# Kernel optimization log

Hardware: AMD Instinct MI355X
Metric: run time of the kernel (lower is better)

The kernel has to match this reference:

```python
import jax, jax.numpy as jnp
import numpy as np

N = 648      # code length (input_size = output_size)
DV = 3       # variable degree
DC = 6       # check degree
M_PER = N // DC            # checks per layer = 108
E = N * DV                 # edges = hidden_size = 1944
BATCH = 2048
CLAMP = 0.999999


def _build_graph():
    rng = np.random.default_rng(0)
    # regular (3,6) Tanner graph via 3 permutation layers
    var_of = np.concatenate([rng.permutation(N) for _ in range(DV)])          # [E]
    chk_of = np.repeat(np.arange(DV * M_PER), DC)                              # [E]
    eye = np.eye(E, dtype=bool)
    same_chk = (chk_of[:, None] == chk_of[None, :]) & ~eye                     # extrinsic same-check
    same_var = (var_of[:, None] == var_of[None, :]) & ~eye                     # extrinsic same-var
    M_ev = np.zeros((E, N), dtype=np.float32)
    M_ev[np.arange(E), var_of] = 1.0                                           # edge -> its variable
    M_first = (same_chk.astype(np.float32) @ M_ev)                             # [E,N] CN extrinsic over vars
    M_cn = same_chk.astype(np.float32)                                         # [E,E] VN2CN_mask_CNUpdate
    M_vn = same_var.astype(np.float32)                                         # [E,E] CN2VN_mask_VNUpdate
    M_out = M_ev.T.copy()                                                      # [N,E] CN2VN_mask_output
    bias_matrix = M_ev.T.copy()                                                # [N,E] dot_bias_matrix
    return M_first, M_cn, M_vn, M_out, bias_matrix


def _xavier(key, out_f, in_f, mask):
    bound = np.sqrt(6.0 / (in_f + out_f)).astype(np.float32)
    w = jax.random.uniform(key, (out_f, in_f), jnp.float32, -bound, bound)
    return w * mask


def setup_inputs() -> dict:
    key = jax.random.key(0)
    M_first, M_cn, M_vn, M_out, bias_matrix = _build_graph()
    M_first = jnp.asarray(M_first); M_cn = jnp.asarray(M_cn)
    M_vn = jnp.asarray(M_vn); M_out = jnp.asarray(M_out)
    bias_matrix = jnp.asarray(bias_matrix)
    ks = jax.random.split(key, 6)
    x = jax.random.normal(ks[0], (BATCH, N), jnp.float32) * 2.0  # channel LLRs
    W1 = _xavier(ks[1], E, E, M_vn)
    W3 = _xavier(ks[2], E, E, M_vn)
    W5 = _xavier(ks[3], E, E, M_vn)
    W7 = _xavier(ks[4], E, E, M_vn)
    W9 = _xavier(ks[5], N, E, M_out)
    B0 = jnp.eye(N, dtype=jnp.float32); B1 = jnp.eye(N, dtype=jnp.float32)
    B2 = jnp.eye(N, dtype=jnp.float32); B3 = jnp.eye(N, dtype=jnp.float32)
    B4 = jnp.eye(N, dtype=jnp.float32)
    return {"x": x, "M_first": M_first, "M_cn": M_cn, "M_out": M_out,
            "bias_matrix": bias_matrix, "W1": W1, "W3": W3, "W5": W5,
            "W7": W7, "W9": W9, "B0": B0, "B1": B1, "B2": B2, "B3": B3, "B4": B4}


def cn_update(x, mask):
    """out[b,i] = prod over j with mask[i,j]!=0 and x[b,j]!=0 of x[b,j]; 0 if none.
    Computed in sign/log domain so it is three dense [B,in]@[in,out] matmuls
    instead of a Python loop over rows."""
    nz = x != 0.0
    logmag = jnp.log(jnp.where(nz, jnp.abs(x), 1.0))          # 0 contribution where x==0
    neg = (x < 0.0).astype(x.dtype)
    log_prod = logmag @ mask.T                                 # [B,out]
    neg_cnt = neg @ mask.T
    sign = 1.0 - 2.0 * jnp.mod(neg_cnt, 2.0)
    any_nz = (nz.astype(x.dtype) @ mask.T) > 0.0
    return jnp.where(any_nz, sign * jnp.exp(log_prod), 0.0)


def reference(x, M_first, M_cn, M_out, bias_matrix, W1, W3, W5, W7, W9,
              B0, B1, B2, B3, B4):
    llr = x                                                    # Channel_LLR [B,N]
    t = jnp.tanh(0.5 * x)
    t = jnp.clip(cn_update(t, M_first), -CLAMP, CLAMP)
    t = 2.0 * jnp.arctanh(t)
    out1 = jax.nn.sigmoid(t @ M_out.T + llr)                   # count_loss_fc: ones*mask weight, zero bias

    t = jnp.tanh(0.5 * (t @ W1.T + (llr @ B0) @ bias_matrix))
    t = jnp.clip(cn_update(t, M_cn), -CLAMP, CLAMP)
    t = 2.0 * jnp.arctanh(t)
    out2 = jax.nn.sigmoid(t @ M_out.T + llr)

    t = jnp.tanh(0.5 * (t @ W3.T + (llr @ B1) @ bias_matrix))
    t = jnp.clip(cn_update(t, M_cn), -CLAMP, CLAMP)
    t = 2.0 * jnp.arctanh(t)
    out3 = jax.nn.sigmoid(t @ M_out.T + llr)

    t = jnp.tanh(0.5 * (t @ W5.T + (llr @ B2) @ bias_matrix))
    t = jnp.clip(cn_update(t, M_cn), -CLAMP, CLAMP)
    t = 2.0 * jnp.arctanh(t)
    out4 = jax.nn.sigmoid(t @ M_out.T + llr)

    t = jnp.tanh(0.5 * (t @ W7.T + (llr @ B3) @ bias_matrix))
    t = jnp.clip(cn_update(t, M_cn), -CLAMP, CLAMP)
    t = 2.0 * jnp.arctanh(t)
    t = t @ W9.T + llr @ B4
    out5 = jax.nn.sigmoid(t)
    return (out5, out4, out3, out2, out1)
```

## Files before the change

kernel.cpp:

```cpp
#include <hip/hip_runtime.h>
#include <math.h>

#define NN 648
#define EE 1944
#define NCHK 324
#define BATCH 2048
#define BS 256
#define BSM 384
#define ROWS 2
#define TL_CLAMP 14.508648f

__device__ __forceinline__ float rcp_fast(float x) { return __builtin_amdgcn_rcpf(x); }

__device__ __forceinline__ float tanh_half(float x) {
    float E = __expf(x);
    float big = 1.0f - 2.0f * rcp_fast(E + 1.0f);
    float u = 0.5f * x;
    float small = u * (1.0f - 0.33333334f * u * u);
    return (fabsf(x) < 0.03125f) ? small : big;
}

__device__ __forceinline__ float sigm(float s) {
    return rcp_fast(1.0f + __expf(-s));
}

__device__ __forceinline__ float cn_edge(float a, float Q) {
    float t = 0.6931472f * (__log2f(fabsf(a + Q)) - __log2f(fabsf(a - Q)));
    return fminf(fmaxf(t, -TL_CLAMP), TL_CLAMP);
}

__device__ __noinline__ float cn_fallback(float a, float t0, float t1, float t2,
                                          float t3, float t4, float t5) {
    float vv[6] = {t0, t1, t2, t3, t4, t5};
    float P = 1.0f; int cz = 0;
    #pragma unroll
    for (int k = 0; k < 6; k++) {
        if (vv[k] == 0.0f) cz++; else P *= vv[k];
    }
    float ext;
    if (a != 0.0f) ext = (cz >= 5) ? 0.0f : P * rcp_fast(a);
    else           ext = (cz >= 6) ? 0.0f : P;
    ext = fminf(fmaxf(ext, -0.999999f), 0.999999f);
    return 0.6931472f * __log2f((1.0f + ext) * rcp_fast(1.0f - ext));
}

__global__ __launch_bounds__(BS) void extract_struct(
    const float4* __restrict__ M_out4,
    int* __restrict__ var_of, int* __restrict__ varEdge) {
    int t = blockIdx.x * BS + threadIdx.x;
    if (t >= NN * EE / 4) return;
    float4 v = M_out4[t];
    int flat = t * 4;
    int n = flat / EE;
    int e = flat - n * EE;
    if (v.x != 0.0f) { var_of[e]     = n; varEdge[n*3 + (e)    /NN] = e;     }
    if (v.y != 0.0f) { var_of[e + 1] = n; varEdge[n*3 + (e + 1)/NN] = e + 1; }
    if (v.z != 0.0f) { var_of[e + 2] = n; varEdge[n*3 + (e + 2)/NN] = e + 2; }
    if (v.w != 0.0f) { var_of[e + 3] = n; varEdge[n*3 + (e + 3)/NN] = e + 3; }
}

__global__ __launch_bounds__(BS) void extract_weights(
    const float* __restrict__ W1, const float* __restrict__ W3,
    const float* __restrict__ W5, const float* __restrict__ W7,
    const float* __restrict__ W9,
    const int* __restrict__ var_of, const int* __restrict__ varEdge,
    unsigned* __restrict__ vnb,
    float4* __restrict__ w1q, float4* __restrict__ w3q,
    float4* __restrict__ w5q, float4* __restrict__ w7q,
    float* __restrict__ w9v) {
    int t = blockIdx.x * BS + threadIdx.x;
    if (t < 4 * EE) {
        int m = t / EE;
        int e = t - m * EE;
        int n = var_of[e];
        int e0 = varEdge[3 * n], e1 = varEdge[3 * n + 1], e2 = varEdge[3 * n + 2];
        int ea, eb;
        if (e == e0)      { ea = e1; eb = e2; }
        else if (e == e1) { ea = e0; eb = e2; }
        else              { ea = e0; eb = e1; }
        const float* W = (m == 0) ? W1 : (m == 1) ? W3 : (m == 2) ? W5 : W7;
        size_t row = (size_t)e * EE;
        float2 w = make_float2(W[row + ea], W[row + eb]);
        float4* dq = (m == 0) ? w1q : (m == 1) ? w3q : (m == 2) ? w5q : w7q;
        ((float2*)dq)[e] = w;
        if (m == 0) vnb[e] = (unsigned)(4 * n + e / NN);
    } else if (t < 4 * EE + NN) {
        int n = t - 4 * EE;
        #pragma unroll
        for (int k = 0; k < 3; k++) {
            int e = varEdge[3 * n + k];
            w9v[3 * n + k] = W9[(size_t)n * EE + e];
        }
    }
}

__global__ __launch_bounds__(BSM, 8) void bp_main(
    const float* __restrict__ x,
    const unsigned* __restrict__ vnb_g,
    const float4* __restrict__ w1q, const float4* __restrict__ w3q,
    const float4* __restrict__ w5q, const float4* __restrict__ w7q,
    const float* __restrict__ w9v,
    float* __restrict__ out) {
    __shared__ __align__(16) float2 llr2[NN];
    __shared__ __align__(16) float2 tlv[4 * NN];
    const int b0 = blockIdx.x * ROWS;
    const int tid = threadIdx.x;

    {
        const float* x0 = x + (size_t)b0 * NN;
        for (int i = tid; i < NN; i += BSM)
            llr2[i] = make_float2(x0[i], x0[NN + i]);
    }
    __syncthreads();

    const bool ck = tid < NCHK;
    const int c = tid;
    float lb0[6], lb1[6];
    float te0[6], te1[6];
    unsigned vb[6];

    if (ck) {
        #pragma unroll
        for (int j = 0; j < 6; j++) {
            vb[j] = vnb_g[6 * c + j];
            float2 l = llr2[vb[j] >> 2];
            lb0[j] = l.x; lb1[j] = l.y;
            te0[j] = tanh_half(lb0[j]);
            te1[j] = tanh_half(lb1[j]);
        }
    }

    auto cn_store = [&]() {
        float Q0 = ((te0[0]*te0[1])*(te0[2]*te0[3]))*(te0[4]*te0[5]);
        float Q1 = ((te1[0]*te1[1])*(te1[2]*te1[3]))*(te1[4]*te1[5]);
        if (__builtin_expect((Q0 != 0.0f) & (Q1 != 0.0f), 1)) {
            #pragma unroll
            for (int j = 0; j < 6; j++)
                tlv[vb[j]] = make_float2(cn_edge(te0[j], Q0),
                                         cn_edge(te1[j], Q1));
        } else {
            #pragma unroll
            for (int j = 0; j < 6; j++) {
                float r0 = (Q0 != 0.0f) ? cn_edge(te0[j], Q0)
                    : cn_fallback(te0[j], te0[0], te0[1], te0[2], te0[3], te0[4], te0[5]);
                float r1 = (Q1 != 0.0f) ? cn_edge(te1[j], Q1)
                    : cn_fallback(te1[j], te1[0], te1[1], te1[2], te1[3], te1[4], te1[5]);
                tlv[vb[j]] = make_float2(r0, r1);
            }
        }
    };
    auto marg = [&](float* dst) {
        #pragma unroll
        for (int j = 0; j < 2; j++) {
            int n = tid + j * BSM;
            if (n < NN) {
                float4 q = *(const float4*)&tlv[4 * n];
                float2 p = tlv[4 * n + 2];
                float2 l = llr2[n];
                dst[n]      = sigm(l.x + (q.x + q.z) + p.x);
                dst[NN + n] = sigm(l.y + (q.y + q.w) + p.y);
            }
        }
    };

    if (ck) cn_store();
    __syncthreads();
    marg(out + ((size_t)(4 * BATCH) + b0) * NN);

    const float4* wqs[4] = {w1q, w3q, w5q, w7q};
    #pragma unroll
    for (int s = 0; s < 4; s++) {
        const float4* __restrict__ wq = wqs[s];
        if (ck) {
            float4 wa = wq[3 * c], wb = wq[3 * c + 1], wc = wq[3 * c + 2];
            float w[12] = {wa.x, wa.y, wa.z, wa.w, wb.x, wb.y, wb.z, wb.w,
                           wc.x, wc.y, wc.z, wc.w};
            #pragma unroll
            for (int j = 0; j < 6; j++) {
                unsigned a = vb[j];
                int k = a & 3;
                const float2* basep = &tlv[a & ~3u];
                float4 q = *(const float4*)basep;
                float2 p = basep[2];
                float cA0 = (k == 0) ? q.z : q.x;
                float cA1 = (k == 0) ? q.w : q.y;
                float cB0 = (k == 2) ? q.z : p.x;
                float cB1 = (k == 2) ? q.w : p.y;
                te0[j] = tanh_half(fmaf(w[2*j], cA0, fmaf(w[2*j+1], cB0, lb0[j])));
                te1[j] = tanh_half(fmaf(w[2*j], cA1, fmaf(w[2*j+1], cB1, lb1[j])));
            }
        }
        __syncthreads();
        if (ck) cn_store();
        __syncthreads();
        if (s < 3) {
            marg(out + ((size_t)((3 - s) * BATCH) + b0) * NN);
        } else {
            #pragma unroll
            for (int j2 = 0; j2 < 2; j2++) {
                int n = tid + j2 * BSM;
                if (n < NN) {
                    float4 q = *(const float4*)&tlv[4 * n];
                    float2 p = tlv[4 * n + 2];
                    float2 l = llr2[n];
                    float u0 = w9v[3*n], u1 = w9v[3*n+1], u2 = w9v[3*n+2];
                    out[(size_t)b0 * NN + n]       = sigm(l.x + u0*q.x + u1*q.z + u2*p.x);
                    out[((size_t)b0 + 1) * NN + n] = sigm(l.y + u0*q.y + u1*q.w + u2*p.y);
                }
            }
        }
    }
}

extern "C" void kernel_launch(void* const* d_in, const int* in_sizes, int n_in,
                              void* d_out, int out_size, void* d_ws, size_t ws_size,
                              hipStream_t stream) {
    const float* x     = (const float*)d_in[0];
    const float* M_out = (const float*)d_in[3];
    const float* W1    = (const float*)d_in[5];
    const float* W3    = (const float*)d_in[6];
    const float* W5    = (const float*)d_in[7];
    const float* W7    = (const float*)d_in[8];
    const float* W9    = (const float*)d_in[9];
    float* out = (float*)d_out;

    char* ws = (char*)d_ws;
    float4* w1q     = (float4*)ws;         ws += (EE / 2) * 16;
    float4* w3q     = (float4*)ws;         ws += (EE / 2) * 16;
    float4* w5q     = (float4*)ws;         ws += (EE / 2) * 16;
    float4* w7q     = (float4*)ws;         ws += (EE / 2) * 16;
    int*    var_of  = (int*)ws;            ws += EE * 4;
    int*    varEdge = (int*)ws;            ws += NN * 3 * 4;
    float*  w9v     = (float*)ws;          ws += NN * 3 * 4;
    unsigned* vnb   = (unsigned*)ws;       ws += EE * 4;

    const int tot4 = NN * EE / 4;
    extract_struct<<<(tot4 + BS - 1) / BS, BS, 0, stream>>>(
        (const float4*)M_out, var_of, varEdge);
    const int totW = 4 * EE + NN;
    extract_weights<<<(totW + BS - 1) / BS, BS, 0, stream>>>(
        W1, W3, W5, W7, W9, var_of, varEdge, vnb, w1q, w3q, w5q, w7q, w9v);
    bp_main<<<BATCH / ROWS, BSM, 0, stream>>>(
        x, vnb, w1q, w3q, w5q, w7q, w9v, out);
}
```

Baseline: 165.6 us.

## Map one batch row to a single 64-thread wavefront per block

Restructures the main decoder kernel from 384-thread blocks handling two batch rows (one check node per thread) to single-wavefront blocks handling one row, each lane looping over six check nodes with 36-element register arrays. Within a single wave, the barriers become cheap and idle threads in the large block are avoided. In exchange, each lane does six times the serial work, register pressure rises sharply, weights are re-read per row instead of shared across two rows, and there are twice as many blocks.

```diff
diff --git a/kernel.cpp b/kernel.cpp
--- a/kernel.cpp
+++ b/kernel.cpp
@@ -6,8 +6,7 @@
 #define NCHK 324
 #define BATCH 2048
 #define BS 256
-#define BSM 384
-#define ROWS 2
+#define BSW 64
 #define TL_CLAMP 14.508648f
 
 __device__ __forceinline__ float rcp_fast(float x) { return __builtin_amdgcn_rcpf(x); }
@@ -94,118 +93,111 @@
     }
 }
 
-__global__ __launch_bounds__(BSM, 8) void bp_main(
+__global__ __launch_bounds__(BSW, 3) void bp_main(
     const float* __restrict__ x,
     const unsigned* __restrict__ vnb_g,
     const float4* __restrict__ w1q, const float4* __restrict__ w3q,
     const float4* __restrict__ w5q, const float4* __restrict__ w7q,
     const float* __restrict__ w9v,
     float* __restrict__ out) {
-    __shared__ __align__(16) float2 llr2[NN];
-    __shared__ __align__(16) float2 tlv[4 * NN];
-    const int b0 = blockIdx.x * ROWS;
-    const int tid = threadIdx.x;
-
-    {
-        const float* x0 = x + (size_t)b0 * NN;
-        for (int i = tid; i < NN; i += BSM)
-            llr2[i] = make_float2(x0[i], x0[NN + i]);
-    }
+    __shared__ float llr_s[NN];
+    __shared__ __align__(16) float tlv[4 * NN];
+    const int b = blockIdx.x;
+    const int lane = threadIdx.x;
+
+    for (int i = lane; i < NN; i += BSW)
+        llr_s[i] = x[(size_t)b * NN + i];
     __syncthreads();
 
-    const bool ck = tid < NCHK;
-    const int c = tid;
-    float lb0[6], lb1[6];
-    float te0[6], te1[6];
-    unsigned vb[6];
-
-    if (ck) {
-        #pragma unroll
-        for (int j = 0; j < 6; j++) {
-            vb[j] = vnb_g[6 * c + j];
-            float2 l = llr2[vb[j] >> 2];
-            lb0[j] = l.x; lb1[j] = l.y;
-            te0[j] = tanh_half(lb0[j]);
-            te1[j] = tanh_half(lb1[j]);
-        }
-    }
-
-    auto cn_store = [&]() {
-        float Q0 = ((te0[0]*te0[1])*(te0[2]*te0[3]))*(te0[4]*te0[5]);
-        float Q1 = ((te1[0]*te1[1])*(te1[2]*te1[3]))*(te1[4]*te1[5]);
-        if (__builtin_expect((Q0 != 0.0f) & (Q1 != 0.0f), 1)) {
+    unsigned vb[36];
+    float te[36];
+
+    #pragma unroll
+    for (int k = 0; k < 6; k++) {
+        int c = lane + 64 * k;
+        if (c < NCHK) {
             #pragma unroll
-            for (int j = 0; j < 6; j++)
-                tlv[vb[j]] = make_float2(cn_edge(te0[j], Q0),
-                                         cn_edge(te1[j], Q1));
+            for (int j = 0; j < 6; j++) {
+                unsigned a = vnb_g[6 * c + j];
+                vb[6 * k + j] = a;
+                te[6 * k + j] = tanh_half(llr_s[a >> 2]);
+            }
+        }
+    }
+
+    auto cn_all = [&]() {
+        #pragma unroll
+        for (int k = 0; k < 6; k++) {
+            int c = lane + 64 * k;
+            if (c < NCHK) {
+                float Q = ((te[6*k] * te[6*k+1]) * (te[6*k+2] * te[6*k+3]))
+                        * (te[6*k+4] * te[6*k+5]);
+                if (__builtin_expect(Q != 0.0f, 1)) {
+                    #pragma unroll
+                    for (int j = 0; j < 6; j++)
+                        tlv[vb[6*k+j]] = cn_edge(te[6*k+j], Q);
+                } else {
+                    #pragma unroll
+                    for (int j = 0; j < 6; j++)
+                        tlv[vb[6*k+j]] = cn_fallback(te[6*k+j],
+                            te[6*k], te[6*k+1], te[6*k+2],
+                            te[6*k+3], te[6*k+4], te[6*k+5]);
+                }
+            }
+        }
+    };
+    auto marg = [&](float* dst) {
+        #pragma unroll
+        for (int i = 0; i < 11; i++) {
+            int n = lane + 64 * i;
+            if (n < NN) {
+                float4 q = *(const float4*)&tlv[4 * n];
+                dst[n] = sigm(llr_s[n] + (q.x + q.y) + q.z);
+            }
+        }
+    };
+
+    cn_all();
+    __syncthreads();
+    marg(out + ((size_t)(4 * BATCH) + b) * NN);
+
+    #pragma unroll 1
+    for (int t = 1; t <= 4; t++) {
+        const float4* __restrict__ wq =
+            (t == 1) ? w1q : (t == 2) ? w3q : (t == 3) ? w5q : w7q;
+        #pragma unroll
+        for (int k = 0; k < 6; k++) {
+            int c = lane + 64 * k;
+            if (c < NCHK) {
+                float4 wa = wq[3 * c], wbv = wq[3 * c + 1], wcv = wq[3 * c + 2];
+                float w[12] = {wa.x, wa.y, wa.z, wa.w, wbv.x, wbv.y, wbv.z, wbv.w,
+                               wcv.x, wcv.y, wcv.z, wcv.w};
+                #pragma unroll
+                for (int j = 0; j < 6; j++) {
+                    unsigned a = vb[6 * k + j];
+                    int kk = a & 3;
+                    float4 q = *(const float4*)&tlv[a & ~3u];
+                    float cA = (kk == 0) ? q.y : q.x;
+                    float cB = (kk == 2) ? q.y : q.z;
+                    float lb = llr_s[a >> 2];
+                    te[6*k+j] = tanh_half(fmaf(w[2*j], cA, fmaf(w[2*j+1], cB, lb)));
+                }
+            }
+        }
+        __syncthreads();
+        cn_all();
+        __syncthreads();
+        if (t < 4) {
+            marg(out + ((size_t)((4 - t) * BATCH) + b) * NN);
         } else {
             #pragma unroll
-            for (int j = 0; j < 6; j++) {
-                float r0 = (Q0 != 0.0f) ? cn_edge(te0[j], Q0)
-                    : cn_fallback(te0[j], te0[0], te0[1], te0[2], te0[3], te0[4], te0[5]);
-                float r1 = (Q1 != 0.0f) ? cn_edge(te1[j], Q1)
-                    : cn_fallback(te1[j], te1[0], te1[1], te1[2], te1[3], te1[4], te1[5]);
-                tlv[vb[j]] = make_float2(r0, r1);
-            }
-        }
-    };
-    auto marg = [&](float* dst) {
-        #pragma unroll
-        for (int j = 0; j < 2; j++) {
-            int n = tid + j * BSM;
-            if (n < NN) {
-                float4 q = *(const float4*)&tlv[4 * n];
-                float2 p = tlv[4 * n + 2];
-                float2 l = llr2[n];
-                dst[n]      = sigm(l.x + (q.x + q.z) + p.x);
-                dst[NN + n] = sigm(l.y + (q.y + q.w) + p.y);
-            }
-        }
-    };
-
-    if (ck) cn_store();
-    __syncthreads();
-    marg(out + ((size_t)(4 * BATCH) + b0) * NN);
-
-    const float4* wqs[4] = {w1q, w3q, w5q, w7q};
-    #pragma unroll
-    for (int s = 0; s < 4; s++) {
-        const float4* __restrict__ wq = wqs[s];
-        if (ck) {
-            float4 wa = wq[3 * c], wb = wq[3 * c + 1], wc = wq[3 * c + 2];
-            float w[12] = {wa.x, wa.y, wa.z, wa.w, wb.x, wb.y, wb.z, wb.w,
-                           wc.x, wc.y, wc.z, wc.w};
-            #pragma unroll
-            for (int j = 0; j < 6; j++) {
-                unsigned a = vb[j];
-                int k = a & 3;
-                const float2* basep = &tlv[a & ~3u];
-                float4 q = *(const float4*)basep;
-                float2 p = basep[2];
-                float cA0 = (k == 0) ? q.z : q.x;
-                float cA1 = (k == 0) ? q.w : q.y;
-                float cB0 = (k == 2) ? q.z : p.x;
-                float cB1 = (k == 2) ? q.w : p.y;
-                te0[j] = tanh_half(fmaf(w[2*j], cA0, fmaf(w[2*j+1], cB0, lb0[j])));
-                te1[j] = tanh_half(fmaf(w[2*j], cA1, fmaf(w[2*j+1], cB1, lb1[j])));
-            }
-        }
-        __syncthreads();
-        if (ck) cn_store();
-        __syncthreads();
-        if (s < 3) {
-            marg(out + ((size_t)((3 - s) * BATCH) + b0) * NN);
-        } else {
-            #pragma unroll
-            for (int j2 = 0; j2 < 2; j2++) {
-                int n = tid + j2 * BSM;
+            for (int i = 0; i < 11; i++) {
+                int n = lane + 64 * i;
                 if (n < NN) {
                     float4 q = *(const float4*)&tlv[4 * n];
-                    float2 p = tlv[4 * n + 2];
-                    float2 l = llr2[n];
-                    float u0 = w9v[3*n], u1 = w9v[3*n+1], u2 = w9v[3*n+2];
-                    out[(size_t)b0 * NN + n]       = sigm(l.x + u0*q.x + u1*q.z + u2*p.x);
-                    out[((size_t)b0 + 1) * NN + n] = sigm(l.y + u0*q.y + u1*q.w + u2*p.y);
+                    float s = llr_s[n] + w9v[3*n] * q.x + w9v[3*n+1] * q.y
+                                       + w9v[3*n+2] * q.z;
+                    out[(size_t)b * NN + n] = sigm(s);
                 }
             }
         }
@@ -240,6 +232,6 @@
     const int totW = 4 * EE + NN;
     extract_weights<<<(totW + BS - 1) / BS, BS, 0, stream>>>(
         W1, W3, W5, W7, W9, var_of, varEdge, vnb, w1q, w3q, w5q, w7q, w9v);
-    bp_main<<<BATCH / ROWS, BSM, 0, stream>>>(
+    bp_main<<<BATCH, BSW, 0, stream>>>(
         x, vnb, w1q, w3q, w5q, w7q, w9v, out);
 }
```

Measured after the change: 198.3 us. 19.7% more time.

## Fuse graph-structure and weight extraction into one kernel; prefetch weights in main loop

Applied to the files above, without the earlier changes.

Merges the two preprocessing kernels into a single kernel in which each wave scans one row of M_out, records that variable's three edges in shared memory, and then gathers the W1/W3/W5/W7/W9 entries directly. This drops one launch and the global var_of/varEdge round trip. In bp_main, the next stage's weights are prefetched into registers one stage ahead, LLR and W9 values are cached in registers, and launch bounds drop from 8 to 6 waves per EU to allow more registers. The trade-off is higher register pressure and possibly lower occupancy.

```diff
diff --git a/kernel.cpp b/kernel.cpp
--- a/kernel.cpp
+++ b/kernel.cpp
@@ -5,7 +5,7 @@
 #define EE 1944
 #define NCHK 324
 #define BATCH 2048
-#define BS 256
+#define BSX 256
 #define BSM 384
 #define ROWS 2
 #define TL_CLAMP 14.508648f
@@ -44,57 +44,62 @@
     return 0.6931472f * __log2f((1.0f + ext) * rcp_fast(1.0f - ext));
 }
 
-__global__ __launch_bounds__(BS) void extract_struct(
+__global__ __launch_bounds__(BSX) void extract_all(
     const float4* __restrict__ M_out4,
-    int* __restrict__ var_of, int* __restrict__ varEdge) {
-    int t = blockIdx.x * BS + threadIdx.x;
-    if (t >= NN * EE / 4) return;
-    float4 v = M_out4[t];
-    int flat = t * 4;
-    int n = flat / EE;
-    int e = flat - n * EE;
-    if (v.x != 0.0f) { var_of[e]     = n; varEdge[n*3 + (e)    /NN] = e;     }
-    if (v.y != 0.0f) { var_of[e + 1] = n; varEdge[n*3 + (e + 1)/NN] = e + 1; }
-    if (v.z != 0.0f) { var_of[e + 2] = n; varEdge[n*3 + (e + 2)/NN] = e + 2; }
-    if (v.w != 0.0f) { var_of[e + 3] = n; varEdge[n*3 + (e + 3)/NN] = e + 3; }
-}
-
-__global__ __launch_bounds__(BS) void extract_weights(
     const float* __restrict__ W1, const float* __restrict__ W3,
     const float* __restrict__ W5, const float* __restrict__ W7,
     const float* __restrict__ W9,
-    const int* __restrict__ var_of, const int* __restrict__ varEdge,
     unsigned* __restrict__ vnb,
-    float4* __restrict__ w1q, float4* __restrict__ w3q,
-    float4* __restrict__ w5q, float4* __restrict__ w7q,
+    float* __restrict__ w1f, float* __restrict__ w3f,
+    float* __restrict__ w5f, float* __restrict__ w7f,
     float* __restrict__ w9v) {
-    int t = blockIdx.x * BS + threadIdx.x;
-    if (t < 4 * EE) {
-        int m = t / EE;
-        int e = t - m * EE;
-        int n = var_of[e];
-        int e0 = varEdge[3 * n], e1 = varEdge[3 * n + 1], e2 = varEdge[3 * n + 2];
-        int ea, eb;
-        if (e == e0)      { ea = e1; eb = e2; }
-        else if (e == e1) { ea = e0; eb = e2; }
-        else              { ea = e0; eb = e1; }
+    const int wave = threadIdx.x >> 6;
+    const int lane = threadIdx.x & 63;
+    const int n = blockIdx.x * (BSX / 64) + wave;
+    __shared__ int varE[BSX / 64][3];
+
+    if (n < NN) {
+        const float4* row = M_out4 + (size_t)n * (EE / 4);
+        #pragma unroll
+        for (int it = 0; it < 8; it++) {
+            int idx = lane + 64 * it;
+            if (idx < EE / 4) {
+                float4 v = row[idx];
+                int e = idx * 4;
+                if (v.x != 0.0f) varE[wave][(e    ) / NN] = e;
+                if (v.y != 0.0f) varE[wave][(e + 1) / NN] = e + 1;
+                if (v.z != 0.0f) varE[wave][(e + 2) / NN] = e + 2;
+                if (v.w != 0.0f) varE[wave][(e + 3) / NN] = e + 3;
+            }
+        }
+    }
+    __syncthreads();
+    if (n >= NN) return;
+    const int e0 = varE[wave][0], e1 = varE[wave][1], e2 = varE[wave][2];
+
+    if (lane < 24) {
+        int m = lane / 6, idx = lane % 6;
+        int k = idx >> 1;
+        int ek = (k == 0) ? e0 : (k == 1) ? e1 : e2;
+        int lo, hi;
+        if (k == 0)      { lo = e1; hi = e2; }
+        else if (k == 1) { lo = e0; hi = e2; }
+        else             { lo = e0; hi = e1; }
+        int eo = (idx & 1) ? hi : lo;
         const float* W = (m == 0) ? W1 : (m == 1) ? W3 : (m == 2) ? W5 : W7;
-        size_t row = (size_t)e * EE;
-        float2 w = make_float2(W[row + ea], W[row + eb]);
-        float4* dq = (m == 0) ? w1q : (m == 1) ? w3q : (m == 2) ? w5q : w7q;
-        ((float2*)dq)[e] = w;
-        if (m == 0) vnb[e] = (unsigned)(4 * n + e / NN);
-    } else if (t < 4 * EE + NN) {
-        int n = t - 4 * EE;
-        #pragma unroll
-        for (int k = 0; k < 3; k++) {
-            int e = varEdge[3 * n + k];
-            w9v[3 * n + k] = W9[(size_t)n * EE + e];
-        }
-    }
-}
-
-__global__ __launch_bounds__(BSM, 8) void bp_main(
+        float v = W[(size_t)ek * EE + eo];
+        float* dst = (m == 0) ? w1f : (m == 1) ? w3f : (m == 2) ? w5f : w7f;
+        dst[2 * ek + (idx & 1)] = v;
+    } else if (lane < 27) {
+        int k = lane - 24;
+        int ek = (k == 0) ? e0 : (k == 1) ? e1 : e2;
+        w9v[3 * n + k] = W9[(size_t)n * EE + ek];
+    } else if (lane == 27) {
+        vnb[e0] = 4u * n + 0; vnb[e1] = 4u * n + 1; vnb[e2] = 4u * n + 2;
+    }
+}
+
+__global__ __launch_bounds__(BSM, 6) void bp_main(
     const float* __restrict__ x,
     const unsigned* __restrict__ vnb_g,
     const float4* __restrict__ w1q, const float4* __restrict__ w3q,
@@ -129,6 +134,14 @@
             te1[j] = tanh_half(lb1[j]);
         }
     }
+    float2 lm[2];
+    #pragma unroll
+    for (int j = 0; j < 2; j++) {
+        int n = tid + j * BSM;
+        lm[j] = (n < NN) ? llr2[n] : make_float2(0.f, 0.f);
+    }
+    float4 wA, wB, wC;
+    if (ck) { wA = w1q[3 * c]; wB = w1q[3 * c + 1]; wC = w1q[3 * c + 2]; }
 
     auto cn_store = [&]() {
         float Q0 = ((te0[0]*te0[1])*(te0[2]*te0[3]))*(te0[4]*te0[5]);
@@ -156,9 +169,8 @@
             if (n < NN) {
                 float4 q = *(const float4*)&tlv[4 * n];
                 float2 p = tlv[4 * n + 2];
-                float2 l = llr2[n];
-                dst[n]      = sigm(l.x + (q.x + q.z) + p.x);
-                dst[NN + n] = sigm(l.y + (q.y + q.w) + p.y);
+                dst[n]      = sigm(lm[j].x + (q.x + q.z) + p.x);
+                dst[NN + n] = sigm(lm[j].y + (q.y + q.w) + p.y);
             }
         }
     };
@@ -168,18 +180,22 @@
     marg(out + ((size_t)(4 * BATCH) + b0) * NN);
 
     const float4* wqs[4] = {w1q, w3q, w5q, w7q};
+    float u0[2], u1[2], u2[2];
     #pragma unroll
     for (int s = 0; s < 4; s++) {
-        const float4* __restrict__ wq = wqs[s];
         if (ck) {
-            float4 wa = wq[3 * c], wb = wq[3 * c + 1], wc = wq[3 * c + 2];
-            float w[12] = {wa.x, wa.y, wa.z, wa.w, wb.x, wb.y, wb.z, wb.w,
-                           wc.x, wc.y, wc.z, wc.w};
+            float4 a = wA, bq = wB, cq = wC;
+            if (s < 3) {
+                const float4* nx = wqs[s + 1];
+                wA = nx[3 * c]; wB = nx[3 * c + 1]; wC = nx[3 * c + 2];
+            }
+            float w[12] = {a.x, a.y, a.z, a.w, bq.x, bq.y, bq.z, bq.w,
+                           cq.x, cq.y, cq.z, cq.w};
             #pragma unroll
             for (int j = 0; j < 6; j++) {
-                unsigned a = vb[j];
-                int k = a & 3;
-                const float2* basep = &tlv[a & ~3u];
+                unsigned ad = vb[j];
+                int k = ad & 3;
+                const float2* basep = &tlv[ad & ~3u];
                 float4 q = *(const float4*)basep;
                 float2 p = basep[2];
                 float cA0 = (k == 0) ? q.z : q.x;
@@ -190,6 +206,16 @@
                 te1[j] = tanh_half(fmaf(w[2*j], cA1, fmaf(w[2*j+1], cB1, lb1[j])));
             }
         }
+        if (s == 3) {
+            #pragma unroll
+            for (int j = 0; j < 2; j++) {
+                int n = tid + j * BSM;
+                if (n < NN) {
+                    u0[j] = w9v[3 * n]; u1[j] = w9v[3 * n + 1];
+                    u2[j] = w9v[3 * n + 2];
+                }
+            }
+        }
         __syncthreads();
         if (ck) cn_store();
         __syncthreads();
@@ -202,10 +228,10 @@
                 if (n < NN) {
                     float4 q = *(const float4*)&tlv[4 * n];
                     float2 p = tlv[4 * n + 2];
-                    float2 l = llr2[n];
-                    float u0 = w9v[3*n], u1 = w9v[3*n+1], u2 = w9v[3*n+2];
-                    out[(size_t)b0 * NN + n]       = sigm(l.x + u0*q.x + u1*q.z + u2*p.x);
-                    out[((size_t)b0 + 1) * NN + n] = sigm(l.y + u0*q.y + u1*q.w + u2*p.y);
+                    out[(size_t)b0 * NN + n] =
+                        sigm(lm[j2].x + u0[j2]*q.x + u1[j2]*q.z + u2[j2]*p.x);
+                    out[((size_t)b0 + 1) * NN + n] =
+                        sigm(lm[j2].y + u0[j2]*q.y + u1[j2]*q.w + u2[j2]*p.y);
                 }
             }
         }
@@ -229,17 +255,12 @@
     float4* w3q     = (float4*)ws;         ws += (EE / 2) * 16;
     float4* w5q     = (float4*)ws;         ws += (EE / 2) * 16;
     float4* w7q     = (float4*)ws;         ws += (EE / 2) * 16;
-    int*    var_of  = (int*)ws;            ws += EE * 4;
-    int*    varEdge = (int*)ws;            ws += NN * 3 * 4;
     float*  w9v     = (float*)ws;          ws += NN * 3 * 4;
     unsigned* vnb   = (unsigned*)ws;       ws += EE * 4;
 
-    const int tot4 = NN * EE / 4;
-    extract_struct<<<(tot4 + BS - 1) / BS, BS, 0, stream>>>(
-        (const float4*)M_out, var_of, varEdge);
-    const int totW = 4 * EE + NN;
-    extract_weights<<<(totW + BS - 1) / BS, BS, 0, stream>>>(
-        W1, W3, W5, W7, W9, var_of, varEdge, vnb, w1q, w3q, w5q, w7q, w9v);
+    extract_all<<<(NN + 3) / 4, BSX, 0, stream>>>(
+        (const float4*)M_out, W1, W3, W5, W7, W9, vnb,
+        (float*)w1q, (float*)w3q, (float*)w5q, (float*)w7q, w9v);
     bp_main<<<BATCH / ROWS, BSM, 0, stream>>>(
         x, vnb, w1q, w3q, w5q, w7q, w9v, out);
 }
```

Result: no change. 167.3 us (+1.0%).
